# Performance work log

Measured on AMD Instinct MI355X. Metric: run time of the kernel, lower is better.

The kernel has to match this reference:

```python
import jax, jax.numpy as jnp
import numpy as np

N_NODES = 100000   # n_nodes
N_EDGES = 1600000  # n_nodes * avg_degree(16)
D_IN = 128
D_OUT = 128


def setup_inputs() -> dict:
    key = jax.random.key(0)
    k1, k2, k3, k4, k5 = jax.random.split(key, 5)
    h = jax.random.normal(k1, (N_NODES, D_IN), dtype=jnp.float32)
    edge_src = jax.random.randint(k2, (N_EDGES,), 0, N_NODES, dtype=jnp.int32)
    edge_dst = jax.random.randint(k3, (N_EDGES,), 0, N_NODES, dtype=jnp.int32)
    # Linear params, init per reset_parameters: U(-stdv, stdv), stdv = 1/sqrt(in_feats)
    stdv = 1.0 / np.sqrt(D_IN)
    W = jax.random.uniform(k4, (D_OUT, D_IN), dtype=jnp.float32, minval=-stdv, maxval=stdv)
    b = jax.random.uniform(k5, (D_OUT,), dtype=jnp.float32, minval=-stdv, maxval=stdv)
    return {"h": h, "edge_src": edge_src, "edge_dst": edge_dst, "W": W, "b": b}


def reference(h, edge_src, edge_dst, W, b):
    # update_all(copy_src('h'), sum) == neighbor-sum aggregation (SpMM with 0/1 adjacency)
    ah = jax.ops.segment_sum(h[edge_src], edge_dst, num_segments=N_NODES)  # [N, D_IN]
    # dense linear + activation fused on the aggregated features
    return jax.nn.relu(ah @ W.T + b)  # [N, D_OUT]
```

## Files before the change

### kernel.cpp

```cpp
#include <hip/hip_runtime.h>

#define D 128
#define BKT_SHIFT 9
#define BKT_SIZE 512
#define P1_EPB 4096
#define CNT_EPB 8192
#define SW_LDU 68

typedef __attribute__((ext_vector_type(8))) short bf16x8;
typedef __attribute__((ext_vector_type(4))) float f32x4;

__device__ inline unsigned int pack2bf(float a, float b) {
    unsigned int ua = __float_as_uint(a);
    unsigned int ub = __float_as_uint(b);
    ua = (ua + 0x7fffu + ((ua >> 16) & 1u)) >> 16;
    ub = (ub + 0x7fffu + ((ub >> 16) & 1u)) >> 16;
    return ua | (ub << 16);
}
__device__ inline unsigned short pack1bf(float a) {
    unsigned int ua = __float_as_uint(a);
    return (unsigned short)((ua + 0x7fffu + ((ua >> 16) & 1u)) >> 16);
}


__global__ __launch_bounds__(256) void bucket_count_kernel(
    const int* __restrict__ edst, int* __restrict__ bucketCnt, int n_edges, int nbk)
{
    __shared__ int hcnt[256];
    const int tid = threadIdx.x;
    hcnt[tid] = 0;
    __syncthreads();
    const int base = blockIdx.x * CNT_EPB;
    const int lim = min(CNT_EPB, n_edges - base);
    for (int k = tid; k < lim; k += 256)
        atomicAdd(&hcnt[edst[base + k] >> BKT_SHIFT], 1);
    __syncthreads();
    if (tid < nbk && hcnt[tid] > 0) atomicAdd(&bucketCnt[tid], hcnt[tid]);
}

__global__ __launch_bounds__(256) void bucket_scan_kernel(
    const int* __restrict__ bucketCnt, int* __restrict__ bucketBase,
    int* __restrict__ bucketCur, int nbk)
{
    __shared__ int s[256];
    const int t = threadIdx.x;
    int v = (t < nbk) ? bucketCnt[t] : 0;
    s[t] = v;
    __syncthreads();
    #pragma unroll
    for (int off = 1; off < 256; off <<= 1) {
        int x = (t >= off) ? s[t - off] : 0;
        __syncthreads();
        s[t] += x;
        __syncthreads();
    }
    if (t < nbk) {
        int base = s[t] - v;
        bucketBase[t] = base;
        bucketCur[t] = base;
    }
}

__global__ __launch_bounds__(256) void p1_partition_kernel(
    const int* __restrict__ esrc, const int* __restrict__ edst,
    int* __restrict__ bucketCur, unsigned int* __restrict__ pairs, int n_edges)
{
    __shared__ int hcnt[256];
    __shared__ int hbase[256];
    const int tid = threadIdx.x;
    const int base = blockIdx.x * P1_EPB;
    hcnt[tid] = 0;
    __syncthreads();
    unsigned int pk[16]; int bk[16];
    #pragma unroll
    for (int k = 0; k < 16; k++) {
        int e = base + k * 256 + tid;
        if (e < n_edges) {
            int sv = esrc[e], dv = edst[e];
            bk[k] = dv >> BKT_SHIFT;
            pk[k] = ((unsigned)sv << BKT_SHIFT) | (unsigned)(dv & (BKT_SIZE - 1));
            atomicAdd(&hcnt[bk[k]], 1);
        } else bk[k] = -1;
    }
    __syncthreads();
    int cval = hcnt[tid];
    if (cval > 0) hbase[tid] = atomicAdd(&bucketCur[tid], cval);
    hcnt[tid] = 0;
    __syncthreads();
    #pragma unroll
    for (int k = 0; k < 16; k++) {
        if (bk[k] >= 0) {
            int loc = atomicAdd(&hcnt[bk[k]], 1);
            pairs[hbase[bk[k]] + loc] = pk[k];
        }
    }
}

__global__ __launch_bounds__(256) void p2_sort_gemm_kernel(
    const unsigned int* __restrict__ pairs, const int* __restrict__ bucketBase,
    int* __restrict__ sorted_src, int* __restrict__ gstart, int* __restrict__ gend,
    const float* __restrict__ h, const float* __restrict__ W,
    unsigned short* __restrict__ z,
    int n_nodes, int n_edges, int nbk)
{
    __shared__ union SU {
        struct { int hist[BKT_SIZE]; int cur[BKT_SIZE]; int sb[256]; } s;
        unsigned int sW[128 * SW_LDU];
    } u;
    const int tid = threadIdx.x;

    if ((int)blockIdx.x < nbk) {
        const int bkt = blockIdx.x;
        const int nbase = bkt << BKT_SHIFT;
        const int pstart = bucketBase[bkt];
        const int pend = (bkt == nbk - 1) ? n_edges : bucketBase[bkt + 1];
        u.s.hist[tid] = 0; u.s.hist[tid + 256] = 0;
        __syncthreads();
        for (int j = pstart + tid; j < pend; j += 256)
            atomicAdd(&u.s.hist[pairs[j] & (BKT_SIZE - 1)], 1);
        __syncthreads();
        int a  = u.s.hist[2 * tid];
        int b2 = u.s.hist[2 * tid + 1];
        int psum = a + b2;
        u.s.sb[tid] = psum;
        __syncthreads();
        #pragma unroll
        for (int off = 1; off < 256; off <<= 1) {
            int x = (tid >= off) ? u.s.sb[tid - off] : 0;
            __syncthreads();
            u.s.sb[tid] += x;
            __syncthreads();
        }
        int pexcl = u.s.sb[tid] - psum;
        u.s.cur[2 * tid] = pexcl;
        u.s.cur[2 * tid + 1] = pexcl + a;
        __syncthreads();
        for (int i = tid; i < BKT_SIZE; i += 256) {
            int nd = nbase + i;
            if (nd < n_nodes) {
                int st = pstart + u.s.cur[i];
                gstart[nd] = st;
                gend[nd] = st + u.s.hist[i];
            }
        }
        __syncthreads();
        for (int j = pstart + tid; j < pend; j += 256) {
            unsigned int p = pairs[j];
            int local = p & (BKT_SIZE - 1);
            int pos = pstart + atomicAdd(&u.s.cur[local], 1);
            sorted_src[pos] = (int)(p >> BKT_SHIFT);
        }
    } else {
        const int gbid = blockIdx.x - nbk;
        for (int i = tid; i < 4096; i += 256) {
            float4 w = ((const float4*)W)[i];
            int row = i >> 5, c4 = i & 31;
            unsigned int* dst = &u.sW[row * SW_LDU + c4 * 2];
            dst[0] = pack2bf(w.x, w.y);
            dst[1] = pack2bf(w.z, w.w);
        }
        __syncthreads();

        const int wave = tid >> 6;
        const int lane = tid & 63;
        const int m = lane & 15;
        const int q = lane >> 4;
        const int r0 = gbid * 64 + wave * 16;
        const int arow = r0 + m;
        const bool rvalid = arow < n_nodes;

        bf16x8 afrag[4];
        #pragma unroll
        for (int ks = 0; ks < 4; ks++) {
            float4 x = make_float4(0.f, 0.f, 0.f, 0.f), y = x;
            if (rvalid) {
                const float4* p = (const float4*)(h + (size_t)arow * D + ks * 32 + q * 8);
                x = p[0]; y = p[1];
            }
            union { unsigned int uu[4]; bf16x8 v; } cvt;
            cvt.uu[0] = pack2bf(x.x, x.y);
            cvt.uu[1] = pack2bf(x.z, x.w);
            cvt.uu[2] = pack2bf(y.x, y.y);
            cvt.uu[3] = pack2bf(y.z, y.w);
            afrag[ks] = cvt.v;
        }

        f32x4 acc[8];
        #pragma unroll
        for (int ct = 0; ct < 8; ct++) acc[ct] = (f32x4){0.f, 0.f, 0.f, 0.f};

        #pragma unroll
        for (int ct = 0; ct < 8; ct++) {
            #pragma unroll
            for (int ks = 0; ks < 4; ks++) {
                const unsigned int* p = &u.sW[(ct * 16 + m) * SW_LDU + ks * 16 + q * 4];
                union { uint4 uu; bf16x8 v; } bu;
                bu.uu = *(const uint4*)p;
                acc[ct] = __builtin_amdgcn_mfma_f32_16x16x32_bf16(afrag[ks], bu.v, acc[ct], 0, 0, 0);
            }
        }

        #pragma unroll
        for (int ct = 0; ct < 8; ct++) {
            int col = ct * 16 + m;
            #pragma unroll
            for (int i = 0; i < 4; i++) {
                int r = r0 + q * 4 + i;
                if (r < n_nodes) z[(size_t)r * D + col] = pack1bf(acc[ct][i]);
            }
        }
    }
}

__global__ __launch_bounds__(256) void p2_sort_kernel(
    const unsigned int* __restrict__ pairs, const int* __restrict__ bucketBase,
    int* __restrict__ sorted_src, int* __restrict__ gstart, int* __restrict__ gend,
    int n_nodes, int n_edges, int nbk)
{
    __shared__ int hist[BKT_SIZE];
    __shared__ int cur[BKT_SIZE];
    __shared__ int sb[256];
    const int tid = threadIdx.x;
    const int bkt = blockIdx.x;
    const int nbase = bkt << BKT_SHIFT;
    const int pstart = bucketBase[bkt];
    const int pend = (bkt == nbk - 1) ? n_edges : bucketBase[bkt + 1];
    hist[tid] = 0; hist[tid + 256] = 0;
    __syncthreads();
    for (int j = pstart + tid; j < pend; j += 256)
        atomicAdd(&hist[pairs[j] & (BKT_SIZE - 1)], 1);
    __syncthreads();
    int a  = hist[2 * tid];
    int b2 = hist[2 * tid + 1];
    int psum = a + b2;
    sb[tid] = psum;
    __syncthreads();
    #pragma unroll
    for (int off = 1; off < 256; off <<= 1) {
        int x = (tid >= off) ? sb[tid - off] : 0;
        __syncthreads();
        sb[tid] += x;
        __syncthreads();
    }
    int pexcl = sb[tid] - psum;
    cur[2 * tid] = pexcl;
    cur[2 * tid + 1] = pexcl + a;
    __syncthreads();
    for (int i = tid; i < BKT_SIZE; i += 256) {
        int nd = nbase + i;
        if (nd < n_nodes) {
            int st = pstart + cur[i];
            gstart[nd] = st;
            gend[nd] = st + hist[i];
        }
    }
    __syncthreads();
    for (int j = pstart + tid; j < pend; j += 256) {
        unsigned int p = pairs[j];
        int local = p & (BKT_SIZE - 1);
        int pos = pstart + atomicAdd(&cur[local], 1);
        sorted_src[pos] = (int)(p >> BKT_SHIFT);
    }
}

__global__ __launch_bounds__(256) void gemm_z_kernel(
    const float* __restrict__ h, const float* __restrict__ W,
    unsigned short* __restrict__ z, int n_nodes)
{
    __shared__ unsigned int sW[128 * SW_LDU];
    const int tid = threadIdx.x;
    for (int i = tid; i < 4096; i += 256) {
        float4 w = ((const float4*)W)[i];
        int row = i >> 5, c4 = i & 31;
        unsigned int* dst = &sW[row * SW_LDU + c4 * 2];
        dst[0] = pack2bf(w.x, w.y);
        dst[1] = pack2bf(w.z, w.w);
    }
    __syncthreads();

    const int wave = tid >> 6;
    const int lane = tid & 63;
    const int m = lane & 15;
    const int q = lane >> 4;
    const int r0 = blockIdx.x * 64 + wave * 16;
    const int arow = r0 + m;
    const bool rvalid = arow < n_nodes;

    bf16x8 afrag[4];
    #pragma unroll
    for (int ks = 0; ks < 4; ks++) {
        float4 x = make_float4(0.f, 0.f, 0.f, 0.f), y = x;
        if (rvalid) {
            const float4* p = (const float4*)(h + (size_t)arow * D + ks * 32 + q * 8);
            x = p[0]; y = p[1];
        }
        union { unsigned int u[4]; bf16x8 v; } cvt;
        cvt.u[0] = pack2bf(x.x, x.y);
        cvt.u[1] = pack2bf(x.z, x.w);
        cvt.u[2] = pack2bf(y.x, y.y);
        cvt.u[3] = pack2bf(y.z, y.w);
        afrag[ks] = cvt.v;
    }

    f32x4 acc[8];
    #pragma unroll
    for (int ct = 0; ct < 8; ct++) acc[ct] = (f32x4){0.f, 0.f, 0.f, 0.f};

    #pragma unroll
    for (int ct = 0; ct < 8; ct++) {
        #pragma unroll
        for (int ks = 0; ks < 4; ks++) {
            const unsigned int* p = &sW[(ct * 16 + m) * SW_LDU + ks * 16 + q * 4];
            union { uint4 u; bf16x8 v; } bu;
            bu.u = *(const uint4*)p;
            acc[ct] = __builtin_amdgcn_mfma_f32_16x16x32_bf16(afrag[ks], bu.v, acc[ct], 0, 0, 0);
        }
    }

    #pragma unroll
    for (int ct = 0; ct < 8; ct++) {
        int col = ct * 16 + m;
        #pragma unroll
        for (int i = 0; i < 4; i++) {
            int r = r0 + q * 4 + i;
            if (r < n_nodes) z[(size_t)r * D + col] = pack1bf(acc[ct][i]);
        }
    }
}

__global__ __launch_bounds__(256) void gather_row_kernel(
    const unsigned short* __restrict__ z, const int* __restrict__ gstart,
    const int* __restrict__ gend, const int* __restrict__ sorted_src,
    const float* __restrict__ b, float* __restrict__ out, int n_nodes)
{
    const int tid = threadIdx.x;
    const int node = blockIdx.x * 16 + (tid >> 4);
    const int lane = tid & 15;
    if (node >= n_nodes) return;
    int e = gstart[node];
    const int end = gend[node];
    const uint4* __restrict__ z4 = (const uint4*)z;
    float acc[8];
    #pragma unroll
    for (int i = 0; i < 8; i++) acc[i] = 0.f;
#define ADDV(v) do { \
    acc[0] += __uint_as_float((v).x << 16); acc[1] += __uint_as_float((v).x & 0xffff0000u); \
    acc[2] += __uint_as_float((v).y << 16); acc[3] += __uint_as_float((v).y & 0xffff0000u); \
    acc[4] += __uint_as_float((v).z << 16); acc[5] += __uint_as_float((v).z & 0xffff0000u); \
    acc[6] += __uint_as_float((v).w << 16); acc[7] += __uint_as_float((v).w & 0xffff0000u); } while (0)
    for (; e + 4 <= end; e += 4) {
        int s0 = sorted_src[e + 0];
        int s1 = sorted_src[e + 1];
        int s2 = sorted_src[e + 2];
        int s3 = sorted_src[e + 3];
        uint4 v0 = z4[(size_t)s0 * 16 + lane];
        uint4 v1 = z4[(size_t)s1 * 16 + lane];
        uint4 v2 = z4[(size_t)s2 * 16 + lane];
        uint4 v3 = z4[(size_t)s3 * 16 + lane];
        ADDV(v0); ADDV(v1); ADDV(v2); ADDV(v3);
    }
    for (; e < end; e++) {
        uint4 v = z4[(size_t)sorted_src[e] * 16 + lane];
        ADDV(v);
    }
#undef ADDV
    float4 b0 = ((const float4*)b)[lane * 2];
    float4 b1 = ((const float4*)b)[lane * 2 + 1];
    float4* o = (float4*)(out + (size_t)node * D + lane * 8);
    o[0] = make_float4(fmaxf(acc[0] + b0.x, 0.f), fmaxf(acc[1] + b0.y, 0.f),
                       fmaxf(acc[2] + b0.z, 0.f), fmaxf(acc[3] + b0.w, 0.f));
    o[1] = make_float4(fmaxf(acc[4] + b1.x, 0.f), fmaxf(acc[5] + b1.y, 0.f),
                       fmaxf(acc[6] + b1.z, 0.f), fmaxf(acc[7] + b1.w, 0.f));
}


__global__ __launch_bounds__(256) void hist_kernel(
    const int* __restrict__ edst, int* __restrict__ cnt, int n_edges)
{
    int gid = blockIdx.x * 256 + threadIdx.x;
    if (gid < n_edges) atomicAdd(&cnt[edst[gid]], 1);
}

__global__ __launch_bounds__(256) void scanA_kernel(
    const int* __restrict__ cnt, int* __restrict__ localoff,
    int* __restrict__ blocksums, int n)
{
    __shared__ int s[256];
    const int t = threadIdx.x;
    const int base = blockIdx.x * 1024 + t * 4;
    int v[4]; int sum = 0;
    #pragma unroll
    for (int i = 0; i < 4; i++) {
        int idx = base + i;
        v[i] = (idx < n) ? cnt[idx] : 0;
        sum += v[i];
    }
    s[t] = sum;
    __syncthreads();
    #pragma unroll
    for (int off = 1; off < 256; off <<= 1) {
        int x = (t >= off) ? s[t - off] : 0;
        __syncthreads();
        s[t] += x;
        __syncthreads();
    }
    int excl = s[t] - sum;
    int run = 0;
    #pragma unroll
    for (int i = 0; i < 4; i++) {
        int idx = base + i;
        if (idx < n) localoff[idx] = excl + run;
        run += v[i];
    }
    if (t == 255) blocksums[blockIdx.x] = s[255];
}

__global__ __launch_bounds__(256) void scanB_kernel(
    const int* __restrict__ blocksums, int* __restrict__ blockoffs, int nb)
{
    __shared__ int s[256];
    const int t = threadIdx.x;
    int v = (t < nb) ? blocksums[t] : 0;
    s[t] = v;
    __syncthreads();
    #pragma unroll
    for (int off = 1; off < 256; off <<= 1) {
        int x = (t >= off) ? s[t - off] : 0;
        __syncthreads();
        s[t] += x;
        __syncthreads();
    }
    if (t < nb) blockoffs[t] = s[t] - v;
}

__global__ __launch_bounds__(256) void scanC_kernel(
    const int* __restrict__ localoff, const int* __restrict__ blockoffs,
    int* __restrict__ outoffs, int* __restrict__ cursor, int n)
{
    int gid = blockIdx.x * 256 + threadIdx.x;
    if (gid >= n) return;
    int v = localoff[gid] + blockoffs[blockIdx.x >> 2];
    outoffs[gid] = v;
    if (cursor) cursor[gid] = v;
}

__global__ __launch_bounds__(256) void place_kernel(
    const int* __restrict__ esrc, const int* __restrict__ edst,
    int* __restrict__ cursor, int* __restrict__ sorted_src, int n_edges)
{
    int gid = blockIdx.x * 256 + threadIdx.x;
    if (gid >= n_edges) return;
    int d = edst[gid];
    int pos = atomicAdd(&cursor[d], 1);
    sorted_src[pos] = esrc[gid];
}

__global__ __launch_bounds__(256) void gather_kernel(
    const float* __restrict__ h, const int* __restrict__ offs,
    const int* __restrict__ endp, const int* __restrict__ sorted_src,
    float* __restrict__ out, int n_nodes)
{
    const int tid = threadIdx.x;
    const int node = blockIdx.x * 8 + (tid >> 5);
    const int lane = tid & 31;
    if (node >= n_nodes) return;
    const int start = offs[node];
    const int end = endp[node];
    const float4* __restrict__ h4 = (const float4*)h;
    float4 acc = make_float4(0.f, 0.f, 0.f, 0.f);
    for (int e = start; e < end; e++) {
        float4 a = h4[(size_t)sorted_src[e] * 32 + lane];
        acc.x += a.x; acc.y += a.y; acc.z += a.z; acc.w += a.w;
    }
    ((float4*)out)[(size_t)node * 32 + lane] = acc;
}

__global__ __launch_bounds__(256) void scatter_kernel(
    const float* __restrict__ h, const int* __restrict__ esrc,
    const int* __restrict__ edst, float* __restrict__ out, int n_edges)
{
    int gid = blockIdx.x * 256 + threadIdx.x;
    int e = gid >> 5;
    int l = gid & 31;
    if (e >= n_edges) return;
    int s = esrc[e];
    int d = edst[e];
    float4 v = ((const float4*)(h + (size_t)s * D))[l];
    float* o = out + (size_t)d * D + (size_t)l * 4;
    atomicAdd(o + 0, v.x);
    atomicAdd(o + 1, v.y);
    atomicAdd(o + 2, v.z);
    atomicAdd(o + 3, v.w);
}

__global__ __launch_bounds__(256) void mfma_gemm_relu_kernel(
    float* __restrict__ io, const float* __restrict__ W,
    const float* __restrict__ b, int n_nodes)
{
    __shared__ unsigned int sW[128 * SW_LDU];
    const int tid = threadIdx.x;
    for (int i = tid; i < 4096; i += 256) {
        float4 w = ((const float4*)W)[i];
        int row = i >> 5, c4 = i & 31;
        unsigned int* dst = &sW[row * SW_LDU + c4 * 2];
        dst[0] = pack2bf(w.x, w.y);
        dst[1] = pack2bf(w.z, w.w);
    }
    __syncthreads();
    const int wave = tid >> 6;
    const int lane = tid & 63;
    const int m = lane & 15;
    const int q = lane >> 4;
    const int r0 = blockIdx.x * 64 + wave * 16;
    const int arow = r0 + m;
    const bool rvalid = arow < n_nodes;
    bf16x8 afrag[4];
    #pragma unroll
    for (int ks = 0; ks < 4; ks++) {
        float4 x = make_float4(0.f, 0.f, 0.f, 0.f), y = x;
        if (rvalid) {
            const float4* p = (const float4*)(io + (size_t)arow * D + ks * 32 + q * 8);
            x = p[0]; y = p[1];
        }
        union { unsigned int u[4]; bf16x8 v; } cvt;
        cvt.u[0] = pack2bf(x.x, x.y);
        cvt.u[1] = pack2bf(x.z, x.w);
        cvt.u[2] = pack2bf(y.x, y.y);
        cvt.u[3] = pack2bf(y.z, y.w);
        afrag[ks] = cvt.v;
    }
    f32x4 acc[8];
    #pragma unroll
    for (int ct = 0; ct < 8; ct++) acc[ct] = (f32x4){0.f, 0.f, 0.f, 0.f};
    #pragma unroll
    for (int ct = 0; ct < 8; ct++) {
        #pragma unroll
        for (int ks = 0; ks < 4; ks++) {
            const unsigned int* p = &sW[(ct * 16 + m) * SW_LDU + ks * 16 + q * 4];
            union { uint4 u; bf16x8 v; } bu;
            bu.u = *(const uint4*)p;
            acc[ct] = __builtin_amdgcn_mfma_f32_16x16x32_bf16(afrag[ks], bu.v, acc[ct], 0, 0, 0);
        }
    }
    #pragma unroll
    for (int ct = 0; ct < 8; ct++) {
        int col = ct * 16 + m;
        float bias = b[col];
        #pragma unroll
        for (int i = 0; i < 4; i++) {
            int r = r0 + q * 4 + i;
            if (r < n_nodes) {
                float v = acc[ct][i] + bias;
                io[(size_t)r * D + col] = v > 0.f ? v : 0.f;
            }
        }
    }
}

extern "C" void kernel_launch(void* const* d_in, const int* in_sizes, int n_in,
                              void* d_out, int out_size, void* d_ws, size_t ws_size,
                              hipStream_t stream) {
    const float* h    = (const float*)d_in[0];
    const int*   esrc = (const int*)d_in[1];
    const int*   edst = (const int*)d_in[2];
    const float* W    = (const float*)d_in[3];
    const float* b    = (const float*)d_in[4];
    float* out = (float*)d_out;
    const int n_nodes = in_sizes[0] / D;
    const int n_edges = in_sizes[1];
    const int NB  = (n_nodes + 1023) / 1024;
    const int NBK = (n_nodes + BKT_SIZE - 1) / BKT_SIZE;

    size_t fixed = ((size_t)2 * n_nodes + 3 * NBK + (size_t)n_edges) * 4;
    size_t pairs_off = (fixed + 15) & ~(size_t)15;
    size_t z_off = (pairs_off + (size_t)n_edges * 4 + 15) & ~(size_t)15;
    size_t need_fused = z_off + (size_t)n_nodes * D * 2;

    size_t zone_bytes = (size_t)n_edges * 4;
    size_t zb2 = (size_t)n_nodes * D * 2;
    if (zb2 > zone_bytes) zone_bytes = zb2;
    size_t need_main = pairs_off + zone_bytes;

    if (ws_size >= need_fused && NBK <= 256 && n_nodes <= (1 << 22)) {
        int* gstart     = (int*)d_ws;
        int* gend       = gstart + n_nodes;
        int* bucketCnt  = gend + n_nodes;
        int* bucketBase = bucketCnt + NBK;
        int* bucketCur  = bucketBase + NBK;
        int* sorted_src = bucketCur + NBK;
        unsigned int* pairs = (unsigned int*)((char*)d_ws + pairs_off);
        unsigned short* z   = (unsigned short*)((char*)d_ws + z_off);

        hipMemsetAsync(bucketCnt, 0, (size_t)NBK * sizeof(int), stream);
        bucket_count_kernel<<<(n_edges + CNT_EPB - 1) / CNT_EPB, 256, 0, stream>>>(
            edst, bucketCnt, n_edges, NBK);
        bucket_scan_kernel<<<1, 256, 0, stream>>>(bucketCnt, bucketBase, bucketCur, NBK);
        p1_partition_kernel<<<(n_edges + P1_EPB - 1) / P1_EPB, 256, 0, stream>>>(
            esrc, edst, bucketCur, pairs, n_edges);
        const int gemmBlocks = (n_nodes + 63) / 64;
        p2_sort_gemm_kernel<<<NBK + gemmBlocks, 256, 0, stream>>>(
            pairs, bucketBase, sorted_src, gstart, gend, h, W, z,
            n_nodes, n_edges, NBK);
        gather_row_kernel<<<(n_nodes + 15) / 16, 256, 0, stream>>>(
            z, gstart, gend, sorted_src, b, out, n_nodes);
        return;
    }

    if (ws_size >= need_main && NBK <= 256 && n_nodes <= (1 << 23)) {
        int* gstart     = (int*)d_ws;
        int* gend       = gstart + n_nodes;
        int* bucketCnt  = gend + n_nodes;
        int* bucketBase = bucketCnt + NBK;
        int* bucketCur  = bucketBase + NBK;
        int* sorted_src = bucketCur + NBK;
        void* zone = (char*)d_ws + pairs_off;
        unsigned int* pairs = (unsigned int*)zone;
        unsigned short* z = (unsigned short*)zone;

        hipMemsetAsync(bucketCnt, 0, (size_t)NBK * sizeof(int), stream);
        bucket_count_kernel<<<(n_edges + CNT_EPB - 1) / CNT_EPB, 256, 0, stream>>>(
            edst, bucketCnt, n_edges, NBK);
        bucket_scan_kernel<<<1, 256, 0, stream>>>(bucketCnt, bucketBase, bucketCur, NBK);
        p1_partition_kernel<<<(n_edges + P1_EPB - 1) / P1_EPB, 256, 0, stream>>>(
            esrc, edst, bucketCur, pairs, n_edges);
        p2_sort_kernel<<<NBK, 256, 0, stream>>>(
            pairs, bucketBase, sorted_src, gstart, gend, n_nodes, n_edges, NBK);
        gemm_z_kernel<<<(n_nodes + 63) / 64, 256, 0, stream>>>(h, W, z, n_nodes);
        gather_row_kernel<<<(n_nodes + 15) / 16, 256, 0, stream>>>(
            z, gstart, gend, sorted_src, b, out, n_nodes);
        return;
    }

    size_t csr_ints = (size_t)3 * n_nodes + 2 * NB + (size_t)n_edges;
    size_t needB = csr_ints * sizeof(int);
    if (ws_size >= needB && NB <= 256) {
        int* cnt        = (int*)d_ws;
        int* offs       = cnt + n_nodes;
        int* cursor     = offs + n_nodes;
        int* blocksums  = cursor + n_nodes;
        int* blockoffs  = blocksums + NB;
        int* sorted_src = blockoffs + NB;

        hipMemsetAsync(cnt, 0, (size_t)n_nodes * sizeof(int), stream);
        hist_kernel<<<(n_edges + 255) / 256, 256, 0, stream>>>(edst, cnt, n_edges);
        scanA_kernel<<<NB, 256, 0, stream>>>(cnt, offs, blocksums, n_nodes);
        scanB_kernel<<<1, 256, 0, stream>>>(blocksums, blockoffs, NB);
        scanC_kernel<<<(n_nodes + 255) / 256, 256, 0, stream>>>(
            offs, blockoffs, cnt, cursor, n_nodes);
        place_kernel<<<(n_edges + 255) / 256, 256, 0, stream>>>(
            esrc, edst, cursor, sorted_src, n_edges);
        gather_kernel<<<(n_nodes + 7) / 8, 256, 0, stream>>>(
            h, cnt, cursor, sorted_src, out, n_nodes);
    } else {
        hipMemsetAsync(out, 0, (size_t)n_nodes * D * sizeof(float), stream);
        long long total = (long long)n_edges * 32;
        scatter_kernel<<<(int)((total + 255) / 256), 256, 0, stream>>>(h, esrc, edst, out, n_edges);
    }
    mfma_gemm_relu_kernel<<<(n_nodes + 63) / 64, 256, 0, stream>>>(out, W, b, n_nodes);
}
```

Baseline: 250.7 us.

## Stage partition writes in LDS, unroll gather by eight, shrink count chunk

The partition kernel now computes a local prefix scan of its bucket histogram and sorts the block's edges into shared memory by bucket. It then writes them to global memory contiguously per bucket, replacing scattered per-element writes. The gather/aggregate kernel unrolls the neighbor loop to 8 loads in flight, with a 2-wide tail loop. CNT_EPB drops from 8192 to 2048, which raises the block count of whatever kernel uses it. Together these add LDS use and extra syncs in exchange for better memory-level parallelism and write coalescing.

```diff
diff --git a/kernel.cpp b/kernel.cpp
--- a/kernel.cpp
+++ b/kernel.cpp
@@ -4,7 +4,7 @@
 #define BKT_SHIFT 9
 #define BKT_SIZE 512
 #define P1_EPB 4096
-#define CNT_EPB 8192
+#define CNT_EPB 2048
 #define SW_LDU 68
 
 typedef __attribute__((ext_vector_type(8))) short bf16x8;
@@ -65,11 +65,15 @@
     const int* __restrict__ esrc, const int* __restrict__ edst,
     int* __restrict__ bucketCur, unsigned int* __restrict__ pairs, int n_edges)
 {
-    __shared__ int hcnt[256];
-    __shared__ int hbase[256];
+    __shared__ int hist[256];
+    __shared__ int lbase[256];
+    __shared__ int gbase[256];
+    __shared__ int cur[256];
+    __shared__ unsigned int buf[P1_EPB];
+    __shared__ unsigned char bkt8[P1_EPB];
     const int tid = threadIdx.x;
     const int base = blockIdx.x * P1_EPB;
-    hcnt[tid] = 0;
+    hist[tid] = 0;
     __syncthreads();
     unsigned int pk[16]; int bk[16];
     #pragma unroll
@@ -79,20 +83,39 @@
             int sv = esrc[e], dv = edst[e];
             bk[k] = dv >> BKT_SHIFT;
             pk[k] = ((unsigned)sv << BKT_SHIFT) | (unsigned)(dv & (BKT_SIZE - 1));
-            atomicAdd(&hcnt[bk[k]], 1);
+            atomicAdd(&hist[bk[k]], 1);
         } else bk[k] = -1;
     }
     __syncthreads();
-    int cval = hcnt[tid];
-    if (cval > 0) hbase[tid] = atomicAdd(&bucketCur[tid], cval);
-    hcnt[tid] = 0;
+    const int v = hist[tid];
+    if (v > 0) gbase[tid] = atomicAdd(&bucketCur[tid], v);
+    lbase[tid] = v;
+    __syncthreads();
+    #pragma unroll
+    for (int off = 1; off < 256; off <<= 1) {
+        int x = (tid >= off) ? lbase[tid - off] : 0;
+        __syncthreads();
+        lbase[tid] += x;
+        __syncthreads();
+    }
+    const int excl = lbase[tid] - v;
+    __syncthreads();
+    lbase[tid] = excl;
+    cur[tid] = excl;
     __syncthreads();
     #pragma unroll
     for (int k = 0; k < 16; k++) {
         if (bk[k] >= 0) {
-            int loc = atomicAdd(&hcnt[bk[k]], 1);
-            pairs[hbase[bk[k]] + loc] = pk[k];
-        }
+            int loc = atomicAdd(&cur[bk[k]], 1);
+            buf[loc] = pk[k];
+            bkt8[loc] = (unsigned char)bk[k];
+        }
+    }
+    __syncthreads();
+    const int total = min(P1_EPB, n_edges - base);
+    for (int i = tid; i < total; i += 256) {
+        int b = bkt8[i];
+        pairs[gbase[b] + (i - lbase[b])] = buf[i];
     }
 }
 
@@ -348,16 +371,32 @@
     acc[2] += __uint_as_float((v).y << 16); acc[3] += __uint_as_float((v).y & 0xffff0000u); \
     acc[4] += __uint_as_float((v).z << 16); acc[5] += __uint_as_float((v).z & 0xffff0000u); \
     acc[6] += __uint_as_float((v).w << 16); acc[7] += __uint_as_float((v).w & 0xffff0000u); } while (0)
-    for (; e + 4 <= end; e += 4) {
+    for (; e + 8 <= end; e += 8) {
         int s0 = sorted_src[e + 0];
         int s1 = sorted_src[e + 1];
         int s2 = sorted_src[e + 2];
         int s3 = sorted_src[e + 3];
+        int s4 = sorted_src[e + 4];
+        int s5 = sorted_src[e + 5];
+        int s6 = sorted_src[e + 6];
+        int s7 = sorted_src[e + 7];
         uint4 v0 = z4[(size_t)s0 * 16 + lane];
         uint4 v1 = z4[(size_t)s1 * 16 + lane];
         uint4 v2 = z4[(size_t)s2 * 16 + lane];
         uint4 v3 = z4[(size_t)s3 * 16 + lane];
+        uint4 v4 = z4[(size_t)s4 * 16 + lane];
+        uint4 v5 = z4[(size_t)s5 * 16 + lane];
+        uint4 v6 = z4[(size_t)s6 * 16 + lane];
+        uint4 v7 = z4[(size_t)s7 * 16 + lane];
         ADDV(v0); ADDV(v1); ADDV(v2); ADDV(v3);
+        ADDV(v4); ADDV(v5); ADDV(v6); ADDV(v7);
+    }
+    for (; e + 2 <= end; e += 2) {
+        int s0 = sorted_src[e + 0];
+        int s1 = sorted_src[e + 1];
+        uint4 v0 = z4[(size_t)s0 * 16 + lane];
+        uint4 v1 = z4[(size_t)s1 * 16 + lane];
+        ADDV(v0); ADDV(v1);
     }
     for (; e < end; e++) {
         uint4 v = z4[(size_t)sorted_src[e] * 16 + lane];
```

Measured after the change: 248.8 us. No clear change (-0.7%).
